# Optimization experiments

Measured on AMD Instinct MI355X. Metric: run time of the kernel, lower is better.

Reference implementation:

```python
import jax, jax.numpy as jnp
import numpy as np

B, H, W, D, C, K, ITERS = 16, 64, 64, 64, 16, 5, 4
EPS_LN = 1e-5

def _ln(x, g, b):
    m = x.mean(-1, keepdims=True)
    v = jnp.mean((x - m) ** 2, axis=-1, keepdims=True)
    return (x - m) / jnp.sqrt(v + EPS_LN) * g + b

def _build_grid(h, w):
    # (h, w, 2) with x in [-1,1] over width, y in [-1,1] over height
    y, x = jnp.meshgrid(jnp.linspace(-1.0, 1.0, h), jnp.linspace(-1.0, 1.0, w), indexing='ij')
    return jnp.stack([x, y], axis=-1)

def _forward(feat, feat_color, mask, slot_noise, slots_mu, slots_logsigma,
             w_grid, b_grid, w_k, w_v, ln_kv_g, ln_kv_b, w_mlp, b_mlp,
             ln_q_g, ln_q_b, w_q, w_ih, w_hh, b_ih, b_hh,
             ln_feat_g, ln_feat_b, ln_color_g, ln_color_b,
             ln_res_g, ln_res_b, w_res, b_res):
    b, h, w, d = feat.shape
    n = h * w
    k_slots = mask.shape[0]
    scale = d ** (-0.5)

    grid = _build_grid(h, w)  # (H, W, 2)

    # fg position: weighted mean of grid under mask -> (K, 2), broadcast to (B, K, 2)
    gm = grid.transpose(2, 0, 1)[None] * mask            # (K, 2, H, W)
    fg_pos = gm.sum((2, 3)) / (mask.sum((2, 3)) + 1e-5)  # (K, 2)
    fg_pos = jnp.broadcast_to(fg_pos[None], (b, k_slots, 2))

    feat_n = _ln(feat.reshape(b, n, d), ln_feat_g, ln_feat_b)                    # (B, N, D)
    featc_n = _ln(feat_color.reshape(b, n, feat_color.shape[-1]), ln_color_g, ln_color_b)

    slot = slots_mu + jnp.exp(slots_logsigma) * slot_noise  # (B, K, D)

    # k/v with relative positional grid embedding (fg_pos is constant across iters,
    # so k/v are iteration-invariant and computed once -- same math as the original loop)
    rel = grid[None, None] - fg_pos[:, :, None, None, :]        # (B, K, H, W, 2)
    rel4 = jnp.concatenate([rel, -rel], -1).reshape(b, k_slots, n, 4)
    grid_embed = rel4 @ w_grid.T + b_grid                       # (B, K, N, D)
    k = _ln(feat_n @ w_k.T[None] [0][None][0][None][0] if False else (feat_n @ w_k.T)[:, None] + grid_embed, ln_kv_g, ln_kv_b) @ w_mlp.T + b_mlp
    v = _ln((feat_n @ w_v.T)[:, None] + grid_embed, ln_kv_g, ln_kv_b) @ w_mlp.T + b_mlp

    attn = None
    for it in range(ITERS):
        prev = slot
        q = _ln(slot, ln_q_g, ln_q_b) @ w_q.T                         # (B, K, D)
        logits = jnp.einsum('bkd,bknd->bkn', q, k) * scale
        attn = jax.nn.softmax(logits, axis=-1)                        # (B, K, N)
        upd = jnp.einsum('bkn,bknd->bkd', attn, v)                    # (B, K, D)
        if it != ITERS - 1:
            # torch GRUCell
            x = upd.reshape(-1, d)
            hp = slot.reshape(-1, d)
            gi = x @ w_ih.T + b_ih
            gh = hp @ w_hh.T + b_hh
            i_r, i_z, i_n = jnp.split(gi, 3, axis=-1)
            h_r, h_z, h_n = jnp.split(gh, 3, axis=-1)
            r = jax.nn.sigmoid(i_r + h_r)
            z = jax.nn.sigmoid(i_z + h_z)
            nn_ = jnp.tanh(i_n + r * h_n)
            slot = ((1.0 - z) * nn_ + z * hp).reshape(b, k_slots, d)
            slot = _ln(slot, ln_res_g, ln_res_b) @ w_res.T + b_res + prev
        else:
            slot_color = jnp.einsum('bkn,bnc->bkc', attn, featc_n)
            slot = jnp.concatenate([slot, slot_color], axis=-1)       # (B, K, D+C)

    amin = attn.min(axis=2, keepdims=True)
    amax = attn.max(axis=2, keepdims=True)
    attn = (attn - amin) / (amax - amin + 1e-5)
    return slot, fg_pos, attn

def setup_inputs() -> dict:
    key = jax.random.key(0)
    ks = jax.random.split(key, 16)
    def rn(i, shape, s=0.02):
        return jax.random.normal(ks[i], shape, jnp.float32) * s
    return {
        'feat': jax.random.normal(ks[0], (B, H, W, D), jnp.float32),
        'feat_color': jax.random.normal(ks[1], (B, H, W, C), jnp.float32),
        'mask': jax.random.uniform(ks[2], (K, 1, H, W), jnp.float32),
        'slot_noise': jax.random.normal(ks[3], (B, K, D), jnp.float32),
        'slots_mu': rn(4, (1, 1, D), 1.0),
        'slots_logsigma': rn(5, (1, 1, D), 0.01),
        'w_grid': rn(6, (D, 4)), 'b_grid': jnp.zeros((D,), jnp.float32),
        'w_k': rn(7, (D, D)), 'w_v': rn(8, (D, D)),
        'ln_kv_g': jnp.ones((D,), jnp.float32), 'ln_kv_b': jnp.zeros((D,), jnp.float32),
        'w_mlp': rn(9, (D, D)), 'b_mlp': jnp.zeros((D,), jnp.float32),
        'ln_q_g': jnp.ones((D,), jnp.float32), 'ln_q_b': jnp.zeros((D,), jnp.float32),
        'w_q': rn(10, (D, D)),
        'w_ih': rn(11, (3 * D, D)), 'w_hh': rn(12, (3 * D, D)),
        'b_ih': jnp.zeros((3 * D,), jnp.float32), 'b_hh': jnp.zeros((3 * D,), jnp.float32),
        'ln_feat_g': jnp.ones((D,), jnp.float32), 'ln_feat_b': jnp.zeros((D,), jnp.float32),
        'ln_color_g': jnp.ones((C,), jnp.float32), 'ln_color_b': jnp.zeros((C,), jnp.float32),
        'ln_res_g': jnp.ones((D,), jnp.float32), 'ln_res_b': jnp.zeros((D,), jnp.float32),
        'w_res': rn(13, (D, D)), 'b_res': jnp.zeros((D,), jnp.float32),
    }

def reference(feat, feat_color, mask, slot_noise, slots_mu, slots_logsigma,
              w_grid, b_grid, w_k, w_v, ln_kv_g, ln_kv_b, w_mlp, b_mlp,
              ln_q_g, ln_q_b, w_q, w_ih, w_hh, b_ih, b_hh,
              ln_feat_g, ln_feat_b, ln_color_g, ln_color_b,
              ln_res_g, ln_res_b, w_res, b_res):
    return _forward(feat, feat_color, mask, slot_noise, slots_mu, slots_logsigma,
                    w_grid, b_grid, w_k, w_v, ln_kv_g, ln_kv_b, w_mlp, b_mlp,
                    ln_q_g, ln_q_b, w_q, w_ih, w_hh, b_ih, b_hh,
                    ln_feat_g, ln_feat_b, ln_color_g, ln_color_b,
                    ln_res_g, ln_res_b, w_res, b_res)
```

## Files before the change

### kernel.cpp

```cpp
#include <hip/hip_runtime.h>
#include <stdint.h>

#define B_ 16
#define H_ 64
#define W_ 64
#define D_ 64
#define C_ 16
#define K_ 5
#define N_ 4096
#define NC_ 16
#define CS_ 256
#define EPS 1e-5f

typedef __attribute__((ext_vector_type(8))) short bf16x8;
typedef __attribute__((ext_vector_type(4))) float f32x4;

__device__ __forceinline__ float wsum64(float v){
  #pragma unroll
  for(int o=1;o<64;o<<=1) v += __shfl_xor(v,o,64);
  return v;
}
__device__ __forceinline__ float wmax64(float v){
  #pragma unroll
  for(int o=1;o<64;o<<=1) v = fmaxf(v, __shfl_xor(v,o,64));
  return v;
}
__device__ __forceinline__ float wmin64(float v){
  #pragma unroll
  for(int o=1;o<64;o<<=1) v = fminf(v, __shfl_xor(v,o,64));
  return v;
}
__device__ __forceinline__ uint16_t f2bf(float f){
  uint32_t u = __float_as_uint(f);
  u += 0x7fffu + ((u>>16)&1u);
  return (uint16_t)(u>>16);
}

__global__ __launch_bounds__(256) void k_pre(
    const float* __restrict__ mask, const float* __restrict__ noise,
    const float* __restrict__ mu, const float* __restrict__ lsg,
    const float* __restrict__ wm, const float* __restrict__ bm, const float* __restrict__ lnkb,
    const float* __restrict__ wk, const float* __restrict__ wv, const float* __restrict__ lnfb,
    const float* __restrict__ wq, const float* __restrict__ lnqg, const float* __restrict__ lnqb,
    const float* __restrict__ wres, const float* __restrict__ bres,
    const float* __restrict__ lnrg, const float* __restrict__ lnrb,
    const float* __restrict__ wih, const float* __restrict__ whh,
    const float* __restrict__ wg, const float* __restrict__ bg,
    float* __restrict__ ws_fg, float* __restrict__ out_fg,
    float* __restrict__ bm2, float* __restrict__ fkb, float* __restrict__ fvb,
    float* __restrict__ qb, float* __restrict__ br2,
    float* __restrict__ wgx, float* __restrict__ wgy, float* __restrict__ gscal,
    float* __restrict__ wqpT, float* __restrict__ wrpT,
    float* __restrict__ wvT, float* __restrict__ wmT,
    float* __restrict__ gw, float* __restrict__ slot){
  int bid=blockIdx.x, tid=threadIdx.x;
  if(bid<5){
    int k=bid;
    float sm=0.f, sx=0.f, sy=0.f;
    for(int p=tid; p<H_*W_; p+=256){
      int i=p>>6, j=p&63;
      float m = mask[k*H_*W_ + p];
      float x = -1.f + (2.f/63.f)*j;
      float y = -1.f + (2.f/63.f)*i;
      sm+=m; sx+=m*x; sy+=m*y;
    }
    __shared__ float r0[4], r1[4], r2[4];
    int wid=tid>>6, lane=tid&63;
    sm=wsum64(sm); sx=wsum64(sx); sy=wsum64(sy);
    if(lane==0){ r0[wid]=sm; r1[wid]=sx; r2[wid]=sy; }
    __syncthreads();
    if(tid==0){
      float tm=r0[0]+r0[1]+r0[2]+r0[3];
      float tx=r1[0]+r1[1]+r1[2]+r1[3];
      float ty=r2[0]+r2[1]+r2[2]+r2[3];
      float px = tx/(tm+1e-5f), py = ty/(tm+1e-5f);
      ws_fg[k*2+0]=px; ws_fg[k*2+1]=py;
      for(int b=0;b<B_;b++){ out_fg[(b*K_+k)*2+0]=px; out_fg[(b*K_+k)*2+1]=py; }
    }
  } else if(bid==5){
    int sel=tid>>6, o=tid&63; float s=0.f;
    if(sel==0){ s=bm[o]; for(int d=0;d<64;d++) s+=lnkb[d]*wm[o*64+d]; bm2[o]=s; }
    else if(sel==1){ for(int d=0;d<64;d++) s+=lnqb[d]*wq[o*64+d]; qb[o]=0.125f*s; }
    else if(sel==2){ for(int d=0;d<64;d++) s+=lnrb[d]*wres[o*64+d]; br2[o]=s+bres[o]; }
    else { for(int d=0;d<64;d++) s+=lnfb[d]*wk[o*64+d]; fkb[o]=s; }
  } else if(bid==6){
    int wv4=tid>>6, l=tid&63;
    if(wv4==0){ float s=0.f; for(int d=0;d<64;d++) s+=lnfb[d]*wv[l*64+d]; fvb[l]=s; }
    else if(wv4==1){
      float4 w4 = *(const float4*)(wg + l*4);
      wgx[l]=w4.x-w4.z; wgy[l]=w4.y-w4.w;
    } else if(wv4==2){
      float4 w4 = *(const float4*)(wg + l*4);
      float wx=w4.x-w4.z, wy=w4.y-w4.w, bl=bg[l];
      float t;
      t=wsum64(wx);    if(l==0) gscal[0]=t*(1.f/64.f);
      t=wsum64(wy);    if(l==0) gscal[1]=t*(1.f/64.f);
      t=wsum64(bl);    if(l==0) gscal[2]=t*(1.f/64.f);
      t=wsum64(wx*wx); if(l==0) gscal[3]=t*(1.f/64.f);
      t=wsum64(wy*wy); if(l==0) gscal[4]=t*(1.f/64.f);
      t=wsum64(wx*wy); if(l==0) gscal[5]=t*(2.f/64.f);
      t=wsum64(wx*bl); if(l==0) gscal[6]=t*(2.f/64.f);
      t=wsum64(wy*bl); if(l==0) gscal[7]=t*(2.f/64.f);
      t=wsum64(bl*bl); if(l==0) gscal[8]=t*(1.f/64.f);
    }
  } else if(bid<71){
    int i=(bid-7)*256+tid;
    int a=i>>12, r=i&4095, d=r>>6, o=r&63;
    if(a==0)      wqpT[r]=0.125f*lnqg[d]*wq[o*64+d];
    else if(a==1) wrpT[r]=lnrg[d]*wres[o*64+d];
    else if(a==2) wvT[r]=wv[o*64+d];
    else          wmT[r]=wm[o*64+d];
  } else if(bid<167){
    int i=(bid-71)*256+tid;
    int g6=i>>12, r=i&4095, d=r>>6, o=r&63;
    float v = (g6<3)? wih[(g6*64+o)*64+d] : whh[((g6-3)*64+o)*64+d];
    gw[g6*4096 + d*64 + o] = v;
  } else {
    int i=(bid-167)*256+tid;
    if(i<B_*K_*D_){ int d=i&63; slot[i]=mu[d]+expf(lsg[d])*noise[i]; }
  }
}

__global__ __launch_bounds__(256) void k_featln(const float* __restrict__ feat,
    const float* __restrict__ wk, const float* __restrict__ wv, const float* __restrict__ gf,
    const float* __restrict__ fkb, const float* __restrict__ fvb,
    const float* __restrict__ wgx, const float* __restrict__ wgy, const float* __restrict__ bg,
    const float* __restrict__ fc, const float* __restrict__ gc, const float* __restrict__ bc,
    uint16_t* __restrict__ Aout, float4* __restrict__ kstat, float4* __restrict__ vstat,
    float* __restrict__ fcn){
  int tid=threadIdx.x, wid=tid>>6, lane=tid&63;
  int q=lane>>4, c=lane&15;
  size_t row = (size_t)blockIdx.x*64 + wid*16 + c;
  const float* xp = feat + row*64;
  float x[16];
  *(float4*)&x[0]  = *(const float4*)(xp + q*8);
  *(float4*)&x[4]  = *(const float4*)(xp + q*8 + 4);
// ... 51 lines not shown
        dx = fmaf(a, wgxl[ot][r], dx);
        dy = fmaf(a, wgyl[ot][r], dy);
        db = fmaf(a, bgl[ot][r], db);
      }
    }
    ss += __shfl_xor(ss,16,64); ss += __shfl_xor(ss,32,64);
    s2 += __shfl_xor(s2,16,64); s2 += __shfl_xor(s2,32,64);
    dx += __shfl_xor(dx,16,64); dx += __shfl_xor(dx,32,64);
    dy += __shfl_xor(dy,16,64); dy += __shfl_xor(dy,32,64);
    db += __shfl_xor(db,16,64); db += __shfl_xor(db,32,64);
    if(lane<16){
      size_t row2 = (size_t)blockIdx.x*64 + wid*16 + lane;
      float4 st = { ss*(1.f/64.f), s2*(1.f/64.f)+db*(1.f/32.f), dx*(1.f/32.f), dy*(1.f/32.f) };
      (mat? vstat : kstat)[row2] = st;
    }
  }
  int r16=tid>>4, cc=tid&15;
  #pragma unroll
  for(int i=0;i<4;i++){
    size_t row2 = (size_t)blockIdx.x*64 + i*16 + r16;
    float xv = fc[row2*16+cc];
    float sc=xv;
    #pragma unroll
    for(int o=1;o<16;o<<=1) sc += __shfl_xor(sc,o,16);
    float m2 = sc*(1.f/16.f);
    float df = xv-m2;
    float v2 = df*df;
    #pragma unroll
    for(int o=1;o<16;o<<=1) v2 += __shfl_xor(v2,o,16);
    fcn[row2*16+cc] = df*rsqrtf(v2*(1.f/16.f)+EPS)*gc[cc] + bc[cc];
  }
}

template<bool GRU>
__global__ __launch_bounds__(256) void k_slotq(
    const float* __restrict__ slot_prev, float* __restrict__ slot_cur,
    const float* __restrict__ part, const float* __restrict__ pscal,
    const float* __restrict__ red_in,
    const float* __restrict__ gw,
    const float* __restrict__ bih, const float* __restrict__ bhh,
    const float* __restrict__ wrpT, const float* __restrict__ br2,
    const float* __restrict__ wqpT, const float* __restrict__ qb,
    const float* __restrict__ wm, const float* __restrict__ wk,
    const float* __restrict__ lnfg, const float* __restrict__ lnkg,
    const float* __restrict__ fkb, const float* __restrict__ bm2, const float* __restrict__ fvb,
    const float* __restrict__ wvT, const float* __restrict__ wmT,
    const float* __restrict__ wgx, const float* __restrict__ wgy, const float* __restrict__ bg,
    const float* __restrict__ gscal,
    float* __restrict__ qs_out, float* __restrict__ cst_out){
  __shared__ float vv[64], vh[64];
  __shared__ float red6[4][64][6];
  int bk=blockIdx.x;
  int tid=threadIdx.x, wid=tid>>6, lane=tid&63;
  int o=lane, qq=wid;
  float mwgx=gscal[0], mwgy=gscal[1], mbg=gscal[2];

  #define MV(Wptr) { float p_=0.f; \
      _Pragma("unroll") \
      for(int dd=0;dd<16;dd++) p_ = fmaf(vv[qq*16+dd], (Wptr)[(qq*16+dd)*64+o], p_); \
      red6[qq][o][0]=p_; } __syncthreads();
  #define SUM0 (red6[0][lane][0]+red6[1][lane][0]+red6[2][lane][0]+red6[3][lane][0])

  float cur=0.f, qv=0.f, qp=0.f, hp=0.f;
  if(GRU){
    float As=0.f, Ax=0.f, Ay=0.f, Am=0.f;
    if(wid==0){
      float mred[NC_], sred[NC_];
      #pragma unroll
      for(int cc=0;cc<NC_;cc++){
        const float* rp = red_in + ((size_t)bk*NC_+cc)*4;
        mred[cc]=rp[0]; sred[cc]=rp[1];
      }
      float M=-1e30f;
      #pragma unroll
      for(int cc=0;cc<NC_;cc++) M=fmaxf(M,mred[cc]);
      float S=0.f;
      #pragma unroll
      for(int cc=0;cc<NC_;cc++){ mred[cc]=__expf(mred[cc]-M); S=fmaf(sred[cc],mred[cc],S); }
      float invS=1.f/S;
      float sA=0.f;
      #pragma unroll
      for(int cc=0;cc<NC_;cc++){
        float lam = mred[cc]*invS;
        sA = fmaf(lam, part[((size_t)bk*NC_+cc)*64+lane], sA);
        const float* pp = pscal + ((size_t)bk*NC_+cc)*4;
        As=fmaf(lam,pp[0],As); Ax=fmaf(lam,pp[1],Ax);
        Ay=fmaf(lam,pp[2],Ay); Am=fmaf(lam,pp[3],Am);
      }
      vv[lane] = lnfg[lane]*sA;
    }
    __syncthreads();
    MV(wvT);
    if(wid==0){
      float fvs = SUM0 + fvb[lane]*As;
      float zs = fvs + Ax*wgx[lane] + Ay*wgy[lane] + As*bg[lane] - Am;
      vv[lane] = lnkg[lane]*zs;
    }
    __syncthreads();
    MV(wmT);
    if(wid==0){
      float x_ = SUM0 + bm2[lane];
      hp = slot_prev[bk*64+lane];
      vv[lane]=x_; vh[lane]=hp;
    }
    __syncthreads();
    {
      float p0=0.f,p1=0.f,p2=0.f,p3=0.f,p4=0.f,p5=0.f;
      #pragma unroll
      for(int dd=0;dd<16;dd++){
        int d = qq*16+dd;
        float xd=vv[d], hd=vh[d];
        p0 = fmaf(xd, gw[d*64+o], p0);
        p1 = fmaf(xd, gw[4096+d*64+o], p1);
        p2 = fmaf(xd, gw[8192+d*64+o], p2);
        p3 = fmaf(hd, gw[12288+d*64+o], p3);
        p4 = fmaf(hd, gw[16384+d*64+o], p4);
        p5 = fmaf(hd, gw[20480+d*64+o], p5);
      }
      red6[qq][o][0]=p0; red6[qq][o][1]=p1; red6[qq][o][2]=p2;
      red6[qq][o][3]=p3; red6[qq][o][4]=p4; red6[qq][o][5]=p5;
    }
    __syncthreads();
    if(wid==0){
      float gir=bih[lane], giz=bih[64+lane], gin=bih[128+lane];
      float ghr=bhh[lane], ghz=bhh[64+lane], ghn=bhh[128+lane];
      #pragma unroll
      for(int w=0;w<4;w++){
        gir+=red6[w][lane][0]; giz+=red6[w][lane][1]; gin+=red6[w][lane][2];
        ghr+=red6[w][lane][3]; ghz+=red6[w][lane][4]; ghn+=red6[w][lane][5];
      }
      float r=1.f/(1.f+__expf(-(gir+ghr)));
      float z=1.f/(1.f+__expf(-(giz+ghz)));
      float nn=tanhf(gin+r*ghn);
      float sp=(1.f-z)*nn+z*hp;
      float m=wsum64(sp)*(1.f/64.f); float df=sp-m;
      float var=wsum64(df*df)*(1.f/64.f);
      vv[lane]=df*rsqrtf(var+EPS);
    }
    __syncthreads();
    MV(wrpT);
    if(wid==0){
      cur = SUM0 + br2[lane] + hp;
      slot_cur[bk*64+lane]=cur;
    }
  } else {
    if(wid==0) cur = slot_prev[bk*64+lane];
  }
  __syncthreads();
  if(wid==0){
    float m=wsum64(cur)*(1.f/64.f); float df=cur-m;
    float var=wsum64(df*df)*(1.f/64.f);
    vv[lane]=df*rsqrtf(var+EPS);
  }
  __syncthreads();
  MV(wqpT);
  if(wid==0){ qv = SUM0 + qb[lane]; vv[lane]=qv; }
  __syncthreads();
  MV(wm);
  if(wid==0){ qp = SUM0*lnkg[lane]; vv[lane]=qp; }
  __syncthreads();
  MV(wk);
  if(wid==0){
    qs_out[bk*64+lane] = SUM0*lnfg[lane];
    float s1 = wsum64(qp);
    float c1 = wsum64(qp*wgx[lane]);
    float c2 = wsum64(qp*wgy[lane]);
    float c3 = wsum64(qp*(bg[lane]+fkb[lane]));
    float c4c = wsum64(qv*bm2[lane]);
    if(lane==0){
      float* cp = cst_out + bk*8;
      cp[0]=c1-s1*mwgx; cp[1]=c2-s1*mwgy; cp[2]=c3-s1*mbg; cp[3]=s1; cp[4]=c4c;
    }
  }
  #undef MV
  #undef SUM0
}

template<bool FINAL>
__global__ __launch_bounds__(256) void k_attn(const uint16_t* __restrict__ Aw,
    const float4* __restrict__ kstat, const float4* __restrict__ vstat,
    const float* __restrict__ qsg, const float* __restrict__ cstg,
    const float* __restrict__ gscal, const float* __restrict__ ws_fg,
    float* __restrict__ lgt, float* __restrict__ red_out,
    float* __restrict__ part_o, float* __restrict__ pscal_o){
  __shared__ uint32_t As_[CS_*32];
  __shared__ float dps[5][CS_+1];
  __shared__ float pw[4][5][64];
  __shared__ float rm[4], rn[4];
  __shared__ float rsc[4][5];
  __shared__ float cstl[5][5];
  __shared__ float fgl[5][2];
  int chunk=blockIdx.x, b=blockIdx.y;
  int tid=threadIdx.x, wid=tid>>6, lane=tid&63;
  int c=lane&15, q=lane>>4;
  float mwgx=gscal[0], mwgy=gscal[1], mbg=gscal[2];
  float g1=gscal[3], g2=gscal[4], g3=gscal[5], g4=gscal[6], g5=gscal[7], g6=gscal[8];

  const uint4* Ag = (const uint4*)(Aw + ((size_t)b*N_ + chunk*CS_)*64);
  #pragma unroll
  for(int jj=0;jj<8;jj++){
    int f = jj*256 + tid;
    uint4 u = Ag[f];
    *(uint4*)(As_ + f*4) = u;
  }
  if(tid<25) cstl[tid/5][tid%5] = cstg[(b*K_ + tid/5)*8 + (tid%5)];
  if(tid>=32 && tid<42){ int i2=tid-32; fgl[i2>>1][i2&1] = ws_fg[i2]; }
  __syncthreads();

  {
    bf16x8 QF0={0,0,0,0,0,0,0,0}, QF1={0,0,0,0,0,0,0,0};
    if(c<5){
      const float* qpp = qsg + (b*K_+c)*64;
      #pragma unroll
      for(int j=0;j<8;j++){
        QF0[j] = (short)f2bf(qpp[q*8+j]);
        QF1[j] = (short)f2bf(qpp[32+q*8+j]);
      }
    }
    const uint16_t* Abase = Aw + ((size_t)b*N_ + chunk*CS_)*64;
    #pragma unroll
    for(int it=0;it<4;it++){
      int tile = wid*64 + it*16;
      const uint16_t* rp = Abase + (size_t)(tile+c)*64;
      bf16x8 BF0 = *(const bf16x8*)(rp + q*8);
      bf16x8 BF1 = *(const bf16x8*)(rp + 32 + q*8);
      f32x4 acc = {0.f,0.f,0.f,0.f};
      acc = __builtin_amdgcn_mfma_f32_16x16x32_bf16(QF0, BF0, acc, 0,0,0);
      acc = __builtin_amdgcn_mfma_f32_16x16x32_bf16(QF1, BF1, acc, 0,0,0);
      #pragma unroll
      for(int r=0;r<4;r++){
        int s = q*4+r;
        if(s<5) dps[s][tile+c]=acc[r];
      }
    }
  }
  __syncthreads();

  int t = tid;
  int n = chunk*CS_ + t;
  float4 st = kstat[(size_t)b*N_ + n];
  float4 sv;
  if(!FINAL) sv = vstat[(size_t)b*N_ + n];
  float gx = -1.f + (2.f/63.f)*(n&63);
  float gy = -1.f + (2.f/63.f)*(n>>6);
  #pragma unroll
  for(int k=0;k<5;k++){
    float rx = gx - fgl[k][0], ry = gy - fgl[k][1];
    float CX=cstl[k][0], CY=cstl[k][1], C0=cstl[k][2], S1=cstl[k][3], C4=cstl[k][4];
    float quad = g1*rx*rx + g2*ry*ry + g3*rx*ry + g4*rx + g5*ry + g6;
    float mu = st.x + rx*mwgx + ry*mwgy + mbg;
    float var = st.y + rx*st.z + ry*st.w + quad - mu*mu;
    float rsn = rsqrtf(var+EPS);
    float l = rsn*(dps[k][t] + rx*CX + ry*CY + C0 - S1*st.x) + C4;
    float wmx = wmax64(l);
    if(lane==0) rm[wid]=wmx;
    if(FINAL){ float mn=wmin64(l); if(lane==0) rn[wid]=mn; }
    __syncthreads();
    float m_c = fmaxf(fmaxf(rm[0],rm[1]),fmaxf(rm[2],rm[3]));
    float e = __expf(l-m_c);
    float scq=e, As2=0.f, Ax2=0.f, Ay2=0.f, Am2=0.f, w_=0.f;
    if(!FINAL){
      float muV = sv.x + rx*mwgx + ry*mwgy + mbg;
      float varV = sv.y + rx*sv.z + ry*sv.w + quad - muV*muV;
      float rsv_ = rsqrtf(varV+EPS);
      w_ = e*rsv_;
      As2=w_; Ax2=w_*rx; Ay2=w_*ry; Am2=w_*muV;
    } else {
      lgt[(size_t)(b*K_+k)*N_ + n] = l;
    }
    scq=wsum64(scq);
    if(!FINAL){ As2=wsum64(As2); Ax2=wsum64(Ax2); Ay2=wsum64(Ay2); Am2=wsum64(Am2); }
    if(lane==0){ rsc[wid][0]=scq; rsc[wid][1]=As2; rsc[wid][2]=Ax2; rsc[wid][3]=Ay2; rsc[wid][4]=Am2; }
    __syncthreads();
    if(tid==0){
      size_t idx = ((size_t)(b*K_+k)*NC_+chunk)*4;
      red_out[idx+0]=m_c;
      red_out[idx+1]=rsc[0][0]+rsc[1][0]+rsc[2][0]+rsc[3][0];
      if(FINAL) red_out[idx+2]=fminf(fminf(rn[0],rn[1]),fminf(rn[2],rn[3]));
      if(!FINAL){
        pscal_o[idx+0]=rsc[0][1]+rsc[1][1]+rsc[2][1]+rsc[3][1];
        pscal_o[idx+1]=rsc[0][2]+rsc[1][2]+rsc[2][2]+rsc[3][2];
        pscal_o[idx+2]=rsc[0][3]+rsc[1][3]+rsc[2][3]+rsc[3][3];
        pscal_o[idx+3]=rsc[0][4]+rsc[1][4]+rsc[2][4]+rsc[3][4];
      }
    }
    if(!FINAL) dps[k][t]=w_;
  }

  if(!FINAL){
    __syncthreads();
    const uint16_t* Au = (const uint16_t*)As_;
    float a[5]={0.f,0.f,0.f,0.f,0.f};
    for(int r64=0;r64<64;r64++){
      int row = wid*64 + r64;
      float av = __uint_as_float(((uint32_t)Au[row*64+lane])<<16);
      #pragma unroll
      for(int k=0;k<5;k++) a[k]=fmaf(dps[k][row], av, a[k]);
    }
    #pragma unroll
    for(int k=0;k<5;k++) pw[wid][k][lane]=a[k];
    __syncthreads();
    if(tid<64){
      #pragma unroll
      for(int k=0;k<5;k++){
        float s2 = pw[0][k][tid]+pw[1][k][tid]+pw[2][k][tid]+pw[3][k][tid];
        part_o[((size_t)(b*K_+k)*NC_+chunk)*64 + tid] = s2;
      }
    }
  }
}

__global__ __launch_bounds__(256) void k_fin(const float* __restrict__ lgt,
    const float* __restrict__ red, const float* __restrict__ featc,
    float* __restrict__ partc, float* __restrict__ out_attn){
  __shared__ float psp[CS_];
  __shared__ float pcz[4][16];
  int chunk=blockIdx.x, bk=blockIdx.y, b=bk/K_;
  int tid=threadIdx.x, wid=tid>>6, lane=tid&63, sub=lane>>4, c4=lane&15;
  const float* rp = red + (size_t)bk*NC_*4;
  float M=-1e30f;
  #pragma unroll
  for(int i=0;i<NC_;i++) M = fmaxf(M, rp[i*4]);
  float S=0.f;
  #pragma unroll
  for(int i=0;i<NC_;i++) S += rp[i*4+1]*__expf(rp[i*4]-M);
  float invS = 1.f/S;
  float LMIN=1e30f;
  #pragma unroll
  for(int i=0;i<NC_;i++) LMIN=fminf(LMIN, rp[i*4+2]);
  float amin = __expf(LMIN-M)*invS;
  float dinv = 1.f/(invS - amin + 1e-5f);
  const float* lp = lgt + (size_t)bk*N_ + chunk*CS_;
  {
    float p = __expf(lp[tid]-M)*invS;
    psp[tid]=p;
    out_attn[(size_t)bk*N_ + chunk*CS_ + tid] = (p - amin)*dinv;
  }
  __syncthreads();
  const float* Fb = featc + ((size_t)b*N_ + chunk*CS_)*16;
  float ac=0.f;
  for(int t=0;t<16;t++){
    int n = wid*64 + t*4 + sub;
    ac += psp[n]*Fb[(size_t)n*16 + c4];
  }
  ac+=__shfl_xor(ac,16,64); ac+=__shfl_xor(ac,32,64);
  if(lane<16) pcz[wid][lane]=ac;
  __syncthreads();
  if(tid<16){
    partc[((size_t)bk*NC_+chunk)*16 + tid] = pcz[0][tid]+pcz[1][tid]+pcz[2][tid]+pcz[3][tid];
  }
}

__global__ __launch_bounds__(64) void k_final(const float* __restrict__ slot,
    const float* __restrict__ partc, float* __restrict__ out_slot){
  int bk=blockIdx.x, lane=threadIdx.x;
  out_slot[bk*80+lane]=slot[bk*64+lane];
  if(lane<16){
    float s=0.f;
    #pragma unroll
    for(int cch=0;cch<NC_;cch++) s += partc[((size_t)bk*NC_+cch)*16+lane];
    out_slot[bk*80+64+lane]=s;
  }
}

extern "C" void kernel_launch(void* const* d_in, const int* in_sizes, int n_in,
                              void* d_out, int out_size, void* d_ws, size_t ws_size,
                              hipStream_t stream){
  (void)in_sizes; (void)n_in; (void)out_size; (void)ws_size;
  const float* feat = (const float*)d_in[0];
  const float* featc= (const float*)d_in[1];
  const float* mask = (const float*)d_in[2];
  const float* noise= (const float*)d_in[3];
  const float* mu   = (const float*)d_in[4];
  const float* lsg  = (const float*)d_in[5];
  const float* wg   = (const float*)d_in[6];
  const float* bg   = (const float*)d_in[7];
  const float* wk   = (const float*)d_in[8];
  const float* wv   = (const float*)d_in[9];
  const float* lnkg = (const float*)d_in[10];
  const float* lnkb = (const float*)d_in[11];
  const float* wm   = (const float*)d_in[12];
  const float* bm   = (const float*)d_in[13];
  const float* lnqg = (const float*)d_in[14];
  const float* lnqb = (const float*)d_in[15];
  const float* wq   = (const float*)d_in[16];
  const float* wih  = (const float*)d_in[17];
  const float* whh  = (const float*)d_in[18];
  const float* bih  = (const float*)d_in[19];
  const float* bhh  = (const float*)d_in[20];
  const float* lnfg = (const float*)d_in[21];
  const float* lnfb = (const float*)d_in[22];
  const float* lncg = (const float*)d_in[23];
  const float* lncb = (const float*)d_in[24];
  const float* lnrg = (const float*)d_in[25];
  const float* lnrb = (const float*)d_in[26];
  const float* wres = (const float*)d_in[27];
  const float* bres = (const float*)d_in[28];

  float* out = (float*)d_out;
  float* out_slot = out;
  float* out_fg   = out + 6400;
  float* out_attn = out + 6560;

  float* wsf     = (float*)d_ws;
  float* ws_fg   = wsf;
  float* ws_bm2  = wsf + 16;
  float* ws_fkb  = ws_bm2 + 64;
  float* ws_fvb  = ws_fkb + 64;
  float* ws_qb   = ws_fvb + 64;
  float* ws_br2  = ws_qb + 64;
  float* ws_wgx  = ws_br2 + 64;
  float* ws_wgy  = ws_wgx + 64;
  float* ws_gs   = ws_wgy + 64;
  float* ws_wqpT = ws_gs + 16;
  float* ws_wrpT = ws_wqpT + 4096;
  float* ws_wvT  = ws_wrpT + 4096;
  float* ws_wmT  = ws_wvT + 4096;
  float* ws_gw   = ws_wmT + 4096;
  float* ws_fc   = ws_gw + 24576;
  float* ws_sl0  = ws_fc + (size_t)B_*N_*C_;
  float* ws_sl1  = ws_sl0 + B_*K_*D_;
  float* ws_qs   = ws_sl1 + B_*K_*D_;
  float* ws_cst  = ws_qs + B_*K_*D_;
  float* ws_lgt  = ws_cst + 640;
  float* ws_red0 = ws_lgt + (size_t)B_*K_*N_;
  float* ws_red1 = ws_red0 + B_*K_*NC_*4;
  float* ws_prt0 = ws_red1 + B_*K_*NC_*4;
  float* ws_prt1 = ws_prt0 + (size_t)B_*K_*NC_*64;
  float* ws_psc0 = ws_prt1 + (size_t)B_*K_*NC_*64;
  float* ws_psc1 = ws_psc0 + B_*K_*NC_*4;
  float* ws_pc   = ws_psc1 + B_*K_*NC_*4;
  float4* ws_kst = (float4*)(ws_pc + B_*K_*NC_*16);
  float4* ws_vst = ws_kst + (size_t)B_*N_;
  uint16_t* ws_A = (uint16_t*)(ws_vst + (size_t)B_*N_);

  k_pre<<<187,256,0,stream>>>(mask,noise,mu,lsg, wm,bm,lnkb, wk,wv,lnfb,
                              wq,lnqg,lnqb, wres,bres,lnrg,lnrb, wih,whh, wg,bg,
                              ws_fg,out_fg, ws_bm2,ws_fkb,ws_fvb,ws_qb,ws_br2,
                              ws_wgx,ws_wgy,ws_gs,
                              ws_wqpT,ws_wrpT,ws_wvT,ws_wmT, ws_gw, ws_sl0);
  k_featln<<<(B_*N_)/64,256,0,stream>>>(feat,wk,wv,lnfg,ws_fkb,ws_fvb,
                                        ws_wgx,ws_wgy,bg,
                                        featc,lncg,lncb,
                                        ws_A,ws_kst,ws_vst,ws_fc);

  dim3 agrid(NC_,B_);
  #define SQ_ARGS(SPREV,SCUR,PIN,SCIN,RIN) SPREV,SCUR,PIN,SCIN,RIN,ws_gw, \
      bih,bhh,ws_wrpT,ws_br2,ws_wqpT,ws_qb, wm,wk,lnfg,lnkg, \
      ws_fkb,ws_bm2,ws_fvb, ws_wvT,ws_wmT, ws_wgx,ws_wgy,bg, ws_gs, ws_qs,ws_cst
  #define AT_ARGS(ROUT,POUT,SCOUT) ws_A,ws_kst,ws_vst,ws_qs,ws_cst,ws_gs,ws_fg, \
      ws_lgt,ROUT,POUT,SCOUT

  k_slotq<false><<<B_*K_,256,0,stream>>>(SQ_ARGS(ws_sl0,ws_sl0,ws_prt1,ws_psc1,ws_red1));
  k_attn<false><<<agrid,256,0,stream>>>(AT_ARGS(ws_red0,ws_prt0,ws_psc0));
  k_slotq<true><<<B_*K_,256,0,stream>>>(SQ_ARGS(ws_sl0,ws_sl1,ws_prt0,ws_psc0,ws_red0));
  k_attn<false><<<agrid,256,0,stream>>>(AT_ARGS(ws_red1,ws_prt1,ws_psc1));
  k_slotq<true><<<B_*K_,256,0,stream>>>(SQ_ARGS(ws_sl1,ws_sl0,ws_prt1,ws_psc1,ws_red1));
  k_attn<false><<<agrid,256,0,stream>>>(AT_ARGS(ws_red0,ws_prt0,ws_psc0));
  k_slotq<true><<<B_*K_,256,0,stream>>>(SQ_ARGS(ws_sl0,ws_sl1,ws_prt0,ws_psc0,ws_red0));
  k_attn<true><<<agrid,256,0,stream>>>(AT_ARGS(ws_red1,ws_prt1,ws_psc1));
  k_fin<<<dim3(NC_,B_*K_),256,0,stream>>>(ws_lgt,ws_red1,ws_fc,ws_pc,out_attn);
  k_final<<<B_*K_,64,0,stream>>>(ws_sl1, ws_pc, out_slot);
}
```

Baseline: 224.0 us.

## Fuse slot GRU/query update into attention kernel and atomically accumulate color output

The per-slot GRU, LayerNorm and query projection work that ran in a separate small kernel is folded into the start of each attention block. Every chunk block now recomputes the update for all five slots of its batch, and only chunk 0 writes the new slot state. The separate final kernel is also removed: colour partials are accumulated into the output with atomicAdd after k_pre zeroes that region. This saves five launches and their inter-kernel gaps, at the cost of 16x redundant small matvec work per iteration and non-deterministic atomic summation order.

```diff
diff --git a/kernel.cpp b/kernel.cpp
--- a/kernel.cpp
+++ b/kernel.cpp
@@ -52,7 +52,7 @@
     float* __restrict__ wgx, float* __restrict__ wgy, float* __restrict__ gscal,
     float* __restrict__ wqpT, float* __restrict__ wrpT,
     float* __restrict__ wvT, float* __restrict__ wmT,
-    float* __restrict__ gw, float* __restrict__ slot){
+    float* __restrict__ gw, float* __restrict__ slot, float* __restrict__ out_slot){
   int bid=blockIdx.x, tid=threadIdx.x;
   if(bid<5){
     int k=bid;
@@ -102,6 +102,8 @@
       t=wsum64(wx*bl); if(l==0) gscal[6]=t*(2.f/64.f);
       t=wsum64(wy*bl); if(l==0) gscal[7]=t*(2.f/64.f);
       t=wsum64(bl*bl); if(l==0) gscal[8]=t*(1.f/64.f);
+    } else {
+      for(int j=l;j<B_*K_*16;j+=64){ int bk2=j>>4, cc2=j&15; out_slot[bk2*80+64+cc2]=0.f; }
     }
   } else if(bid<71){
     int i=(bid-7)*256+tid;
@@ -219,195 +221,247 @@
   }
 }
 
-template<bool GRU>
-__global__ __launch_bounds__(256) void k_slotq(
-    const float* __restrict__ slot_prev, float* __restrict__ slot_cur,
-    const float* __restrict__ part, const float* __restrict__ pscal,
+struct AttnP {
+  const uint16_t* Aw; const float4* kst; const float4* vst;
+  const float* gw; const float* bih; const float* bhh;
+  const float* wrpT; const float* br2; const float* wqpT; const float* qb;
+  const float* wm; const float* wk; const float* lnfg; const float* lnkg;
+  const float* fkb; const float* bm2; const float* fvb;
+  const float* wvT; const float* wmT;
+  const float* wgx; const float* wgy; const float* bg;
+  const float* gs; const float* fg; float* lgt;
+};
+
+template<bool GRU, bool FINAL>
+__global__ __launch_bounds__(256) void k_attn(AttnP P,
+    const float* __restrict__ sprev, float* __restrict__ scur,
+    const float* __restrict__ prt_in, const float* __restrict__ psc_in,
     const float* __restrict__ red_in,
-    const float* __restrict__ gw,
-    const float* __restrict__ bih, const float* __restrict__ bhh,
-    const float* __restrict__ wrpT, const float* __restrict__ br2,
-    const float* __restrict__ wqpT, const float* __restrict__ qb,
-    const float* __restrict__ wm, const float* __restrict__ wk,
-    const float* __restrict__ lnfg, const float* __restrict__ lnkg,
-    const float* __restrict__ fkb, const float* __restrict__ bm2, const float* __restrict__ fvb,
-    const float* __restrict__ wvT, const float* __restrict__ wmT,
-    const float* __restrict__ wgx, const float* __restrict__ wgy, const float* __restrict__ bg,
-    const float* __restrict__ gscal,
-    float* __restrict__ qs_out, float* __restrict__ cst_out){
-  __shared__ float vv[64], vh[64];
-  __shared__ float red6[4][64][6];
-  int bk=blockIdx.x;
-  int tid=threadIdx.x, wid=tid>>6, lane=tid&63;
-  int o=lane, qq=wid;
-  float mwgx=gscal[0], mwgy=gscal[1], mbg=gscal[2];
-
-  #define MV(Wptr) { float p_=0.f; \
-      _Pragma("unroll") \
-      for(int dd=0;dd<16;dd++) p_ = fmaf(vv[qq*16+dd], (Wptr)[(qq*16+dd)*64+o], p_); \
-      red6[qq][o][0]=p_; } __syncthreads();
-  #define SUM0 (red6[0][lane][0]+red6[1][lane][0]+red6[2][lane][0]+red6[3][lane][0])
-
-  float cur=0.f, qv=0.f, qp=0.f, hp=0.f;
-  if(GRU){
-    float As=0.f, Ax=0.f, Ay=0.f, Am=0.f;
-    if(wid==0){
-      float mred[NC_], sred[NC_];
-      #pragma unroll
-      for(int cc=0;cc<NC_;cc++){
-        const float* rp = red_in + ((size_t)bk*NC_+cc)*4;
-        mred[cc]=rp[0]; sred[cc]=rp[1];
-      }
-      float M=-1e30f;
-      #pragma unroll
-      for(int cc=0;cc<NC_;cc++) M=fmaxf(M,mred[cc]);
-      float S=0.f;
-      #pragma unroll
-      for(int cc=0;cc<NC_;cc++){ mred[cc]=__expf(mred[cc]-M); S=fmaf(sred[cc],mred[cc],S); }
-      float invS=1.f/S;
-      float sA=0.f;
-      #pragma unroll
-      for(int cc=0;cc<NC_;cc++){
-        float lam = mred[cc]*invS;
-        sA = fmaf(lam, part[((size_t)bk*NC_+cc)*64+lane], sA);
-        const float* pp = pscal + ((size_t)bk*NC_+cc)*4;
-        As=fmaf(lam,pp[0],As); Ax=fmaf(lam,pp[1],Ax);
-        Ay=fmaf(lam,pp[2],Ay); Am=fmaf(lam,pp[3],Am);
-      }
-      vv[lane] = lnfg[lane]*sA;
-    }
-    __syncthreads();
-    MV(wvT);
-    if(wid==0){
-      float fvs = SUM0 + fvb[lane]*As;
-      float zs = fvs + Ax*wgx[lane] + Ay*wgy[lane] + As*bg[lane] - Am;
-      vv[lane] = lnkg[lane]*zs;
-    }
-    __syncthreads();
-    MV(wmT);
-    if(wid==0){
-      float x_ = SUM0 + bm2[lane];
-      hp = slot_prev[bk*64+lane];
-      vv[lane]=x_; vh[lane]=hp;
-    }
-    __syncthreads();
-    {
-      float p0=0.f,p1=0.f,p2=0.f,p3=0.f,p4=0.f,p5=0.f;
-      #pragma unroll
-      for(int dd=0;dd<16;dd++){
-        int d = qq*16+dd;
-        float xd=vv[d], hd=vh[d];
-        p0 = fmaf(xd, gw[d*64+o], p0);
-        p1 = fmaf(xd, gw[4096+d*64+o], p1);
-        p2 = fmaf(xd, gw[8192+d*64+o], p2);
-        p3 = fmaf(hd, gw[12288+d*64+o], p3);
-        p4 = fmaf(hd, gw[16384+d*64+o], p4);
-        p5 = fmaf(hd, gw[20480+d*64+o], p5);
-      }
-      red6[qq][o][0]=p0; red6[qq][o][1]=p1; red6[qq][o][2]=p2;
-      red6[qq][o][3]=p3; red6[qq][o][4]=p4; red6[qq][o][5]=p5;
-    }
-    __syncthreads();
-    if(wid==0){
-      float gir=bih[lane], giz=bih[64+lane], gin=bih[128+lane];
-      float ghr=bhh[lane], ghz=bhh[64+lane], ghn=bhh[128+lane];
-      #pragma unroll
-      for(int w=0;w<4;w++){
-        gir+=red6[w][lane][0]; giz+=red6[w][lane][1]; gin+=red6[w][lane][2];
-        ghr+=red6[w][lane][3]; ghz+=red6[w][lane][4]; ghn+=red6[w][lane][5];
-      }
-      float r=1.f/(1.f+__expf(-(gir+ghr)));
-      float z=1.f/(1.f+__expf(-(giz+ghz)));
-      float nn=tanhf(gin+r*ghn);
-      float sp=(1.f-z)*nn+z*hp;
-      float m=wsum64(sp)*(1.f/64.f); float df=sp-m;
-      float var=wsum64(df*df)*(1.f/64.f);
-      vv[lane]=df*rsqrtf(var+EPS);
-    }
-    __syncthreads();
-    MV(wrpT);
-    if(wid==0){
-      cur = SUM0 + br2[lane] + hp;
-      slot_cur[bk*64+lane]=cur;
-    }
-  } else {
-    if(wid==0) cur = slot_prev[bk*64+lane];
-  }
-  __syncthreads();
-  if(wid==0){
-    float m=wsum64(cur)*(1.f/64.f); float df=cur-m;
-    float var=wsum64(df*df)*(1.f/64.f);
-    vv[lane]=df*rsqrtf(var+EPS);
-  }
-  __syncthreads();
-  MV(wqpT);
-  if(wid==0){ qv = SUM0 + qb[lane]; vv[lane]=qv; }
-  __syncthreads();
-  MV(wm);
-  if(wid==0){ qp = SUM0*lnkg[lane]; vv[lane]=qp; }
-  __syncthreads();
-  MV(wk);
-  if(wid==0){
-    qs_out[bk*64+lane] = SUM0*lnfg[lane];
-    float s1 = wsum64(qp);
-    float c1 = wsum64(qp*wgx[lane]);
-    float c2 = wsum64(qp*wgy[lane]);
-    float c3 = wsum64(qp*(bg[lane]+fkb[lane]));
-    float c4c = wsum64(qv*bm2[lane]);
-    if(lane==0){
-      float* cp = cst_out + bk*8;
-      cp[0]=c1-s1*mwgx; cp[1]=c2-s1*mwgy; cp[2]=c3-s1*mbg; cp[3]=s1; cp[4]=c4c;
-    }
-  }
-  #undef MV
-  #undef SUM0
-}
-
-template<bool FINAL>
-__global__ __launch_bounds__(256) void k_attn(const uint16_t* __restrict__ Aw,
-    const float4* __restrict__ kstat, const float4* __restrict__ vstat,
-    const float* __restrict__ qsg, const float* __restrict__ cstg,
-    const float* __restrict__ gscal, const float* __restrict__ ws_fg,
-    float* __restrict__ lgt, float* __restrict__ red_out,
-    float* __restrict__ part_o, float* __restrict__ pscal_o){
+    float* __restrict__ red_out, float* __restrict__ prt_out, float* __restrict__ psc_out){
   __shared__ uint32_t As_[CS_*32];
-  __shared__ float dps[5][CS_+1];
-  __shared__ float pw[4][5][64];
+  __shared__ float dps[5][CS_+4];
+  __shared__ float scratch[4][64][15];
+  __shared__ float vvs[5][64], vh[5][64], qsl[5][64];
+  __shared__ float scal5[5][4];
+  __shared__ float cstl[5][5];
+  __shared__ float fgl[5][2];
   __shared__ float rm[4], rn[4];
   __shared__ float rsc[4][5];
-  __shared__ float cstl[5][5];
-  __shared__ float fgl[5][2];
   int chunk=blockIdx.x, b=blockIdx.y;
   int tid=threadIdx.x, wid=tid>>6, lane=tid&63;
   int c=lane&15, q=lane>>4;
-  float mwgx=gscal[0], mwgy=gscal[1], mbg=gscal[2];
-  float g1=gscal[3], g2=gscal[4], g3=gscal[5], g4=gscal[6], g5=gscal[7], g6=gscal[8];
-
-  const uint4* Ag = (const uint4*)(Aw + ((size_t)b*N_ + chunk*CS_)*64);
+  int o=lane, qq=wid;
+  float mwgx=P.gs[0], mwgy=P.gs[1], mbg=P.gs[2];
+  float g1=P.gs[3], g2=P.gs[4], g3=P.gs[5], g4=P.gs[6], g5=P.gs[7], g6=P.gs[8];
+
+  const uint4* Ag = (const uint4*)(P.Aw + ((size_t)b*N_ + chunk*CS_)*64);
   #pragma unroll
   for(int jj=0;jj<8;jj++){
     int f = jj*256 + tid;
-    uint4 u = Ag[f];
-    *(uint4*)(As_ + f*4) = u;
-  }
-  if(tid<25) cstl[tid/5][tid%5] = cstg[(b*K_ + tid/5)*8 + (tid%5)];
-  if(tid>=32 && tid<42){ int i2=tid-32; fgl[i2>>1][i2&1] = ws_fg[i2]; }
+    *(uint4*)(As_ + f*4) = Ag[f];
+  }
+  if(tid<10) fgl[tid>>1][tid&1] = P.fg[tid];
+  int nrow = chunk*CS_ + tid;
+  float4 st = P.kst[(size_t)b*N_ + nrow];
+  float4 sv;
+  if(!FINAL) sv = P.vst[(size_t)b*N_ + nrow];
+  float gx = -1.f + (2.f/63.f)*(nrow&63);
+  float gy = -1.f + (2.f/63.f)*(nrow>>6);
+
+  #define MV5(W) { float p0=0.f,p1=0.f,p2=0.f,p3=0.f,p4=0.f; \
+    _Pragma("unroll") \
+    for(int dd=0;dd<16;dd++){ int d_=qq*16+dd; float w_=(W)[d_*64+o]; \
+      p0=fmaf(vvs[0][d_],w_,p0); p1=fmaf(vvs[1][d_],w_,p1); \
+      p2=fmaf(vvs[2][d_],w_,p2); p3=fmaf(vvs[3][d_],w_,p3); \
+      p4=fmaf(vvs[4][d_],w_,p4); } \
+    scratch[qq][o][0]=p0; scratch[qq][o][1]=p1; scratch[qq][o][2]=p2; \
+    scratch[qq][o][3]=p3; scratch[qq][o][4]=p4; } __syncthreads();
+  #define SUM5(k) (scratch[0][lane][k]+scratch[1][lane][k]+scratch[2][lane][k]+scratch[3][lane][k])
+
+  if(GRU){
+    #pragma unroll
+    for(int rd=0;rd<2;rd++){
+      int k = (rd==0)? wid : (wid==0? 4 : -1);
+      if(k>=0 && k<5){
+        int bk=b*K_+k;
+        float mred[NC_], sred[NC_];
+        float M=-1e30f;
+        #pragma unroll
+        for(int cc=0;cc<NC_;cc++){
+          const float* rp = red_in + ((size_t)bk*NC_+cc)*4;
+          mred[cc]=rp[0]; sred[cc]=rp[1];
+          M=fmaxf(M,mred[cc]);
+        }
+        float S=0.f;
+        #pragma unroll
+        for(int cc=0;cc<NC_;cc++){ mred[cc]=__expf(mred[cc]-M); S=fmaf(sred[cc],mred[cc],S); }
+        float invS=1.f/S;
+        float sA=0.f, As=0.f, Ax=0.f, Ay=0.f, Am=0.f;
+        #pragma unroll
+        for(int cc=0;cc<NC_;cc++){
+          float lam = mred[cc]*invS;
+          sA = fmaf(lam, prt_in[((size_t)bk*NC_+cc)*64+lane], sA);
+          const float* pp = psc_in + ((size_t)bk*NC_+cc)*4;
+          As=fmaf(lam,pp[0],As); Ax=fmaf(lam,pp[1],Ax);
+          Ay=fmaf(lam,pp[2],Ay); Am=fmaf(lam,pp[3],Am);
+        }
+        vvs[k][lane] = P.lnfg[lane]*sA;
+        if(lane==0){ scal5[k][0]=As; scal5[k][1]=Ax; scal5[k][2]=Ay; scal5[k][3]=Am; }
+      }
+    }
+    __syncthreads();
+    MV5(P.wvT);
+    if(wid==0){
+      #pragma unroll
+      for(int k=0;k<5;k++){
+        float As=scal5[k][0],Ax=scal5[k][1],Ay=scal5[k][2],Am=scal5[k][3];
+        float fvs = SUM5(k) + P.fvb[lane]*As;
+        float zs = fvs + Ax*P.wgx[lane] + Ay*P.wgy[lane] + As*P.bg[lane] - Am;
+        vvs[k][lane] = P.lnkg[lane]*zs;
+      }
+    }
+    __syncthreads();
+    MV5(P.wmT);
+    if(wid==0){
+      #pragma unroll
+      for(int k=0;k<5;k++){
+        vh[k][lane] = sprev[(b*K_+k)*64+lane];
+        vvs[k][lane] = SUM5(k) + P.bm2[lane];
+      }
+    }
+    __syncthreads();
+    {
+      float p[15];
+      #pragma unroll
+      for(int i=0;i<15;i++) p[i]=0.f;
+      #pragma unroll
+      for(int dd=0;dd<16;dd++){
+        int d_=qq*16+dd;
+        float w0=P.gw[d_*64+o], w1=P.gw[4096+d_*64+o], w2=P.gw[8192+d_*64+o];
+        #pragma unroll
+        for(int k=0;k<5;k++){
+          float xd=vvs[k][d_];
+          p[k]=fmaf(xd,w0,p[k]); p[5+k]=fmaf(xd,w1,p[5+k]); p[10+k]=fmaf(xd,w2,p[10+k]);
+        }
+      }
+      #pragma unroll
+      for(int i=0;i<15;i++) scratch[qq][o][i]=p[i];
+    }
+    __syncthreads();
+    float gA[15];
+    if(wid==0){
+      #pragma unroll
+      for(int i=0;i<15;i++) gA[i]=scratch[0][lane][i]+scratch[1][lane][i]+scratch[2][lane][i]+scratch[3][lane][i];
+    }
+    __syncthreads();
+    {
+      float p[15];
+      #pragma unroll
+      for(int i=0;i<15;i++) p[i]=0.f;
+      #pragma unroll
+      for(int dd=0;dd<16;dd++){
+        int d_=qq*16+dd;
+        float w0=P.gw[12288+d_*64+o], w1=P.gw[16384+d_*64+o], w2=P.gw[20480+d_*64+o];
+        #pragma unroll
+        for(int k=0;k<5;k++){
+          float hd=vh[k][d_];
+          p[k]=fmaf(hd,w0,p[k]); p[5+k]=fmaf(hd,w1,p[5+k]); p[10+k]=fmaf(hd,w2,p[10+k]);
+        }
+      }
+      #pragma unroll
+      for(int i=0;i<15;i++) scratch[qq][o][i]=p[i];
+    }
+    __syncthreads();
+    if(wid==0){
+      float gB[15];
+      #pragma unroll
+      for(int i=0;i<15;i++) gB[i]=scratch[0][lane][i]+scratch[1][lane][i]+scratch[2][lane][i]+scratch[3][lane][i];
+      float b0=P.bih[lane], b1=P.bih[64+lane], b2=P.bih[128+lane];
+      float h0=P.bhh[lane], h1=P.bhh[64+lane], h2=P.bhh[128+lane];
+      #pragma unroll
+      for(int k=0;k<5;k++){
+        float gir=gA[k]+b0, giz=gA[5+k]+b1, gin=gA[10+k]+b2;
+        float ghr=gB[k]+h0, ghz=gB[5+k]+h1, ghn=gB[10+k]+h2;
+        float r=1.f/(1.f+__expf(-(gir+ghr)));
+        float z=1.f/(1.f+__expf(-(giz+ghz)));
+        float nn=tanhf(gin+r*ghn);
+        float hp=vh[k][lane];
+        float sp=(1.f-z)*nn+z*hp;
+        float m=wsum64(sp)*(1.f/64.f); float df=sp-m;
+        float var=wsum64(df*df)*(1.f/64.f);
+        vvs[k][lane]=df*rsqrtf(var+EPS);
+      }
+    }
+    __syncthreads();
+    MV5(P.wrpT);
+    if(wid==0){
+      #pragma unroll
+      for(int k=0;k<5;k++){
+        float cur = SUM5(k) + P.br2[lane] + vh[k][lane];
+        if(chunk==0) scur[(b*K_+k)*64+lane]=cur;
+        float m=wsum64(cur)*(1.f/64.f); float df=cur-m;
+        float var=wsum64(df*df)*(1.f/64.f);
+        vvs[k][lane]=df*rsqrtf(var+EPS);
+      }
+    }
+  } else {
+    if(wid==0){
+      #pragma unroll
+      for(int k=0;k<5;k++){
+        float cur = sprev[(b*K_+k)*64+lane];
+        float m=wsum64(cur)*(1.f/64.f); float df=cur-m;
+        float var=wsum64(df*df)*(1.f/64.f);
+        vvs[k][lane]=df*rsqrtf(var+EPS);
+      }
+    }
+  }
   __syncthreads();
+  MV5(P.wqpT);
+  if(wid==0){
+    #pragma unroll
+    for(int k=0;k<5;k++){ float qv=SUM5(k)+P.qb[lane]; vh[k][lane]=qv; vvs[k][lane]=qv; }
+  }
+  __syncthreads();
+  MV5(P.wm);
+  if(wid==0){
+    #pragma unroll
+    for(int k=0;k<5;k++){ float qp=SUM5(k)*P.lnkg[lane]; dps[k][lane]=qp; vvs[k][lane]=qp; }
+  }
+  __syncthreads();
+  MV5(P.wk);
+  if(wid==0){
+    #pragma unroll
+    for(int k=0;k<5;k++){
+      qsl[k][lane]=SUM5(k)*P.lnfg[lane];
+      float qp=dps[k][lane], qv=vh[k][lane];
+      float s1 = wsum64(qp);
+      float c1 = wsum64(qp*P.wgx[lane]);
+      float c2 = wsum64(qp*P.wgy[lane]);
+      float c3 = wsum64(qp*(P.bg[lane]+P.fkb[lane]));
+      float c4c = wsum64(qv*P.bm2[lane]);
+      if(lane==0){
+        cstl[k][0]=c1-s1*mwgx; cstl[k][1]=c2-s1*mwgy; cstl[k][2]=c3-s1*mbg;
+        cstl[k][3]=s1; cstl[k][4]=c4c;
+      }
+    }
+  }
+  __syncthreads();
+  #undef MV5
+  #undef SUM5
 
   {
     bf16x8 QF0={0,0,0,0,0,0,0,0}, QF1={0,0,0,0,0,0,0,0};
     if(c<5){
-      const float* qpp = qsg + (b*K_+c)*64;
       #pragma unroll
       for(int j=0;j<8;j++){
-        QF0[j] = (short)f2bf(qpp[q*8+j]);
-        QF1[j] = (short)f2bf(qpp[32+q*8+j]);
-      }
-    }
-    const uint16_t* Abase = Aw + ((size_t)b*N_ + chunk*CS_)*64;
-    #pragma unroll
-    for(int it=0;it<4;it++){
-      int tile = wid*64 + it*16;
+        QF0[j] = (short)f2bf(qsl[c][q*8+j]);
+        QF1[j] = (short)f2bf(qsl[c][32+q*8+j]);
+      }
+    }
+    const uint16_t* Abase = P.Aw + ((size_t)b*N_ + chunk*CS_)*64;
+    #pragma unroll
+    for(int it2=0;it2<4;it2++){
+      int tile = wid*64 + it2*16;
       const uint16_t* rp = Abase + (size_t)(tile+c)*64;
       bf16x8 BF0 = *(const bf16x8*)(rp + q*8);
       bf16x8 BF1 = *(const bf16x8*)(rp + 32 + q*8);
@@ -423,13 +477,6 @@
   }
   __syncthreads();
 
-  int t = tid;
-  int n = chunk*CS_ + t;
-  float4 st = kstat[(size_t)b*N_ + n];
-  float4 sv;
-  if(!FINAL) sv = vstat[(size_t)b*N_ + n];
-  float gx = -1.f + (2.f/63.f)*(n&63);
-  float gy = -1.f + (2.f/63.f)*(n>>6);
   #pragma unroll
   for(int k=0;k<5;k++){
     float rx = gx - fgl[k][0], ry = gy - fgl[k][1];
@@ -438,7 +485,7 @@
     float mu = st.x + rx*mwgx + ry*mwgy + mbg;
     float var = st.y + rx*st.z + ry*st.w + quad - mu*mu;
     float rsn = rsqrtf(var+EPS);
-    float l = rsn*(dps[k][t] + rx*CX + ry*CY + C0 - S1*st.x) + C4;
+    float l = rsn*(dps[k][tid] + rx*CX + ry*CY + C0 - S1*st.x) + C4;
     float wmx = wmax64(l);
     if(lane==0) rm[wid]=wmx;
     if(FINAL){ float mn=wmin64(l); if(lane==0) rn[wid]=mn; }
@@ -453,7 +500,7 @@
       w_ = e*rsv_;
       As2=w_; Ax2=w_*rx; Ay2=w_*ry; Am2=w_*muV;
     } else {
-      lgt[(size_t)(b*K_+k)*N_ + n] = l;
+      P.lgt[(size_t)(b*K_+k)*N_ + nrow] = l;
     }
     scq=wsum64(scq);
     if(!FINAL){ As2=wsum64(As2); Ax2=wsum64(Ax2); Ay2=wsum64(Ay2); Am2=wsum64(Am2); }
@@ -465,13 +512,13 @@
       red_out[idx+1]=rsc[0][0]+rsc[1][0]+rsc[2][0]+rsc[3][0];
       if(FINAL) red_out[idx+2]=fminf(fminf(rn[0],rn[1]),fminf(rn[2],rn[3]));
       if(!FINAL){
-        pscal_o[idx+0]=rsc[0][1]+rsc[1][1]+rsc[2][1]+rsc[3][1];
-        pscal_o[idx+1]=rsc[0][2]+rsc[1][2]+rsc[2][2]+rsc[3][2];
-        pscal_o[idx+2]=rsc[0][3]+rsc[1][3]+rsc[2][3]+rsc[3][3];
-        pscal_o[idx+3]=rsc[0][4]+rsc[1][4]+rsc[2][4]+rsc[3][4];
-      }
-    }
-    if(!FINAL) dps[k][t]=w_;
+        psc_out[idx+0]=rsc[0][1]+rsc[1][1]+rsc[2][1]+rsc[3][1];
+        psc_out[idx+1]=rsc[0][2]+rsc[1][2]+rsc[2][2]+rsc[3][2];
+        psc_out[idx+2]=rsc[0][3]+rsc[1][3]+rsc[2][3]+rsc[3][3];
+        psc_out[idx+3]=rsc[0][4]+rsc[1][4]+rsc[2][4]+rsc[3][4];
+      }
+    }
+    if(!FINAL) dps[k][tid]=w_;
   }
 
   if(!FINAL){
@@ -485,13 +532,13 @@
       for(int k=0;k<5;k++) a[k]=fmaf(dps[k][row], av, a[k]);
     }
     #pragma unroll
-    for(int k=0;k<5;k++) pw[wid][k][lane]=a[k];
+    for(int k=0;k<5;k++) scratch[wid][lane][k]=a[k];
     __syncthreads();
     if(tid<64){
       #pragma unroll
       for(int k=0;k<5;k++){
-        float s2 = pw[0][k][tid]+pw[1][k][tid]+pw[2][k][tid]+pw[3][k][tid];
-        part_o[((size_t)(b*K_+k)*NC_+chunk)*64 + tid] = s2;
+        float s2 = scratch[0][tid][k]+scratch[1][tid][k]+scratch[2][tid][k]+scratch[3][tid][k];
+        prt_out[((size_t)(b*K_+k)*NC_+chunk)*64 + tid] = s2;
       }
     }
   }
@@ -499,7 +546,8 @@
 
 __global__ __launch_bounds__(256) void k_fin(const float* __restrict__ lgt,
     const float* __restrict__ red, const float* __restrict__ featc,
-    float* __restrict__ partc, float* __restrict__ out_attn){
+    const float* __restrict__ sl1, float* __restrict__ out_slot,
+    float* __restrict__ out_attn){
   __shared__ float psp[CS_];
   __shared__ float pcz[4][16];
   int chunk=blockIdx.x, bk=blockIdx.y, b=bk/K_;
@@ -534,20 +582,10 @@
   if(lane<16) pcz[wid][lane]=ac;
   __syncthreads();
   if(tid<16){
-    partc[((size_t)bk*NC_+chunk)*16 + tid] = pcz[0][tid]+pcz[1][tid]+pcz[2][tid]+pcz[3][tid];
-  }
-}
-
-__global__ __launch_bounds__(64) void k_final(const float* __restrict__ slot,
-    const float* __restrict__ partc, float* __restrict__ out_slot){
-  int bk=blockIdx.x, lane=threadIdx.x;
-  out_slot[bk*80+lane]=slot[bk*64+lane];
-  if(lane<16){
-    float s=0.f;
-    #pragma unroll
-    for(int cch=0;cch<NC_;cch++) s += partc[((size_t)bk*NC_+cch)*16+lane];
-    out_slot[bk*80+64+lane]=s;
-  }
+    float s2 = pcz[0][tid]+pcz[1][tid]+pcz[2][tid]+pcz[3][tid];
+    atomicAdd(&out_slot[bk*80+64+tid], s2);
+  }
+  if(chunk==0 && tid<64) out_slot[bk*80+tid]=sl1[bk*64+tid];
 }
 
 extern "C" void kernel_launch(void* const* d_in, const int* in_sizes, int n_in,
@@ -607,17 +645,14 @@
   float* ws_fc   = ws_gw + 24576;
   float* ws_sl0  = ws_fc + (size_t)B_*N_*C_;
   float* ws_sl1  = ws_sl0 + B_*K_*D_;
-  float* ws_qs   = ws_sl1 + B_*K_*D_;
-  float* ws_cst  = ws_qs + B_*K_*D_;
-  float* ws_lgt  = ws_cst + 640;
+  float* ws_lgt  = ws_sl1 + B_*K_*D_;
   float* ws_red0 = ws_lgt + (size_t)B_*K_*N_;
   float* ws_red1 = ws_red0 + B_*K_*NC_*4;
   float* ws_prt0 = ws_red1 + B_*K_*NC_*4;
   float* ws_prt1 = ws_prt0 + (size_t)B_*K_*NC_*64;
   float* ws_psc0 = ws_prt1 + (size_t)B_*K_*NC_*64;
   float* ws_psc1 = ws_psc0 + B_*K_*NC_*4;
-  float* ws_pc   = ws_psc1 + B_*K_*NC_*4;
-  float4* ws_kst = (float4*)(ws_pc + B_*K_*NC_*16);
+  float4* ws_kst = (float4*)(ws_psc1 + B_*K_*NC_*4);
   float4* ws_vst = ws_kst + (size_t)B_*N_;
   uint16_t* ws_A = (uint16_t*)(ws_vst + (size_t)B_*N_);
 
@@ -625,27 +660,30 @@
                               wq,lnqg,lnqb, wres,bres,lnrg,lnrb, wih,whh, wg,bg,
                               ws_fg,out_fg, ws_bm2,ws_fkb,ws_fvb,ws_qb,ws_br2,
                               ws_wgx,ws_wgy,ws_gs,
-                              ws_wqpT,ws_wrpT,ws_wvT,ws_wmT, ws_gw, ws_sl0);
+                              ws_wqpT,ws_wrpT,ws_wvT,ws_wmT, ws_gw, ws_sl0, out_slot);
   k_featln<<<(B_*N_)/64,256,0,stream>>>(feat,wk,wv,lnfg,ws_fkb,ws_fvb,
                                         ws_wgx,ws_wgy,bg,
                                         featc,lncg,lncb,
                                         ws_A,ws_kst,ws_vst,ws_fc);
 
+  AttnP P;
+  P.Aw=ws_A; P.kst=ws_kst; P.vst=ws_vst;
+  P.gw=ws_gw; P.bih=bih; P.bhh=bhh;
+  P.wrpT=ws_wrpT; P.br2=ws_br2; P.wqpT=ws_wqpT; P.qb=ws_qb;
+  P.wm=wm; P.wk=wk; P.lnfg=lnfg; P.lnkg=lnkg;
+  P.fkb=ws_fkb; P.bm2=ws_bm2; P.fvb=ws_fvb;
+  P.wvT=ws_wvT; P.wmT=ws_wmT;
+  P.wgx=ws_wgx; P.wgy=ws_wgy; P.bg=bg;
+  P.gs=ws_gs; P.fg=ws_fg; P.lgt=ws_lgt;
+
   dim3 agrid(NC_,B_);
-  #define SQ_ARGS(SPREV,SCUR,PIN,SCIN,RIN) SPREV,SCUR,PIN,SCIN,RIN,ws_gw, \
-      bih,bhh,ws_wrpT,ws_br2,ws_wqpT,ws_qb, wm,wk,lnfg,lnkg, \
-      ws_fkb,ws_bm2,ws_fvb, ws_wvT,ws_wmT, ws_wgx,ws_wgy,bg, ws_gs, ws_qs,ws_cst
-  #define AT_ARGS(ROUT,POUT,SCOUT) ws_A,ws_kst,ws_vst,ws_qs,ws_cst,ws_gs,ws_fg, \
-      ws_lgt,ROUT,POUT,SCOUT
-
-  k_slotq<false><<<B_*K_,256,0,stream>>>(SQ_ARGS(ws_sl0,ws_sl0,ws_prt1,ws_psc1,ws_red1));
-  k_attn<false><<<agrid,256,0,stream>>>(AT_ARGS(ws_red0,ws_prt0,ws_psc0));
-  k_slotq<true><<<B_*K_,256,0,stream>>>(SQ_ARGS(ws_sl0,ws_sl1,ws_prt0,ws_psc0,ws_red0));
-  k_attn<false><<<agrid,256,0,stream>>>(AT_ARGS(ws_red1,ws_prt1,ws_psc1));
-  k_slotq<true><<<B_*K_,256,0,stream>>>(SQ_ARGS(ws_sl1,ws_sl0,ws_prt1,ws_psc1,ws_red1));
-  k_attn<false><<<agrid,256,0,stream>>>(AT_ARGS(ws_red0,ws_prt0,ws_psc0));
-  k_slotq<true><<<B_*K_,256,0,stream>>>(SQ_ARGS(ws_sl0,ws_sl1,ws_prt0,ws_psc0,ws_red0));
-  k_attn<true><<<agrid,256,0,stream>>>(AT_ARGS(ws_red1,ws_prt1,ws_psc1));
-  k_fin<<<dim3(NC_,B_*K_),256,0,stream>>>(ws_lgt,ws_red1,ws_fc,ws_pc,out_attn);
-  k_final<<<B_*K_,64,0,stream>>>(ws_sl1, ws_pc, out_slot);
-}
+  k_attn<false,false><<<agrid,256,0,stream>>>(P, ws_sl0, ws_sl0,
+      ws_prt1, ws_psc1, ws_red1, ws_red0, ws_prt0, ws_psc0);
+  k_attn<true,false><<<agrid,256,0,stream>>>(P, ws_sl0, ws_sl1,
+      ws_prt0, ws_psc0, ws_red0, ws_red1, ws_prt1, ws_psc1);
+  k_attn<true,false><<<agrid,256,0,stream>>>(P, ws_sl1, ws_sl0,
+      ws_prt1, ws_psc1, ws_red1, ws_red0, ws_prt0, ws_psc0);
+  k_attn<true,true><<<agrid,256,0,stream>>>(P, ws_sl0, ws_sl1,
+      ws_prt0, ws_psc0, ws_red0, ws_red1, ws_prt1, ws_psc1);
+  k_fin<<<dim3(NC_,B_*K_),256,0,stream>>>(ws_lgt,ws_red1,ws_fc,ws_sl1,out_slot,out_attn);
+}
```

New measurement: 255.2 us. 1.14x slower.
